# Kernel tuning notes

Hardware: AMD Instinct MI355X
Metric: run time of the kernel (lower is better)

Reference implementation:

```python
import jax, jax.numpy as jnp
import numpy as np

N = 2048      # nodes
E = 65536     # edges (avg degree 32)
IN_C = 512
OUT_C = 512
KP1 = 3       # K=2 Chebyshev -> 3 terms


def setup_inputs() -> dict:
    key = jax.random.key(0)
    k0, k1, k2, k3, k4 = jax.random.split(key, 5)
    X_real = jax.random.normal(k0, (N, IN_C), jnp.float32)
    X_imag = jax.random.normal(k1, (N, IN_C), jnp.float32)
    edges = jax.random.randint(k2, (2, E), 0, N).astype(jnp.int64)
    edge_weight = jax.random.uniform(k3, (E,), jnp.float32)
    q = jnp.float32(0.25)
    stdv = 1.0 / np.sqrt(OUT_C)
    weight = jax.random.uniform(k4, (KP1, IN_C, OUT_C), jnp.float32, -stdv, stdv)
    bias = jnp.zeros((1, OUT_C), jnp.float32)
    return {"X_real": X_real, "X_imag": X_imag, "edges": edges, "q": q,
            "edge_weight": edge_weight, "weight": weight, "bias": bias}


def _cheb_laplacians(edges, edge_weight, q):
    """QinDirect_hermitian_decomp_sparse (norm=True, laplacian=True, max_eigen=2,
    gcn_appr=False) followed by cheb_poly_sparse with K=2. Returns stacked
    real/imag parts of [T0, T1, T2], each [KP1, N, N]."""
    f, e = edges[0], edges[1]
    A = jnp.zeros((N, N), jnp.float32).at[f, e].add(edge_weight)
    A_sym = 0.5 * (A + A.T)
    deg = A_sym.sum(axis=0)
    dinv = jnp.where(deg == 0.0, 1.0, deg) ** -0.5
    A_norm = dinv[:, None] * A_sym * dinv[None, :]   # D^-1/2 A_sym D^-1/2
    theta = (2.0 * jnp.pi) * q * (A - A.T)           # phase matrix
    # L = I - exp(i*theta) .* A_norm ; scaled (2/max_eigen)*L - I with max_eigen=2
    # => L_scaled = -exp(i*theta) .* A_norm
    L1_re = -jnp.cos(theta) * A_norm
    L1_im = -jnp.sin(theta) * A_norm
    eye = jnp.eye(N, dtype=jnp.float32)
    # T2 = 2*L1@L1 - I (complex square in real arithmetic)
    L2_re = 2.0 * (L1_re @ L1_re - L1_im @ L1_im) - eye
    L2_im = 2.0 * (L1_re @ L1_im + L1_im @ L1_re)
    L_re = jnp.stack([eye, L1_re, L2_re])                        # [KP1,N,N]
    L_im = jnp.stack([jnp.zeros((N, N), jnp.float32), L1_im, L2_im])
    return L_re, L_im


def reference(X_real, X_imag, edges, q, edge_weight, weight, bias):
    L_re, L_im = _cheb_laplacians(edges, edge_weight, q)
    # NOTE: original forward swaps the lists: L_norm_real = L_img, L_norm_imag = L_real.
    mr, mi = L_im, L_re
    # per term k: real_k = (mr_k@Xr - mi_k@Xi) @ W_k ; imag_k = (mi_k@Xr + mr_k@Xi) @ W_k
    Ar = jnp.einsum('knm,mf->knf', mr, X_real) - jnp.einsum('knm,mf->knf', mi, X_imag)
    Ai = jnp.einsum('knm,mf->knf', mi, X_real) + jnp.einsum('knm,mf->knf', mr, X_imag)
    real = jnp.einsum('knf,kfo->no', Ar, weight)   # sum over K terms
    imag = jnp.einsum('knf,kfo->no', Ai, weight)
    return real + bias, imag + bias
```

## Files before the change

kernel.cpp:

```cpp
#include <hip/hip_runtime.h>
#include <hip/hip_bf16.h>
#include <math.h>

#define NN 2048
#define CC 512
#define NEDGE 65536

typedef __hip_bfloat16 bf16;
typedef __attribute__((ext_vector_type(8))) short short8;
typedef __attribute__((ext_vector_type(4))) float floatx4;

static constexpr float TWO_PI_F = 6.2831853071795864769f;

__device__ __forceinline__ void gld16(const void* g, void* l) {
    __builtin_amdgcn_global_load_lds(
        (const __attribute__((address_space(1))) unsigned int*)(unsigned long long)(uintptr_t)g,
        (__attribute__((address_space(3))) unsigned int*)(unsigned long long)(uintptr_t)l,
        16, 0, 0);
}

__global__ __launch_bounds__(256) void detect_k(const unsigned int* __restrict__ qword,
                                                const unsigned int* __restrict__ ewords,
                                                int* __restrict__ flag,
                                                float* __restrict__ colsum) {
    int tid = threadIdx.x;
#pragma unroll
    for (int i = 0; i < 8; ++i) colsum[tid * 8 + i] = 0.f;
    if (tid < 64) {
        unsigned int w0 = ewords[2 * tid + 1];
        unsigned int w1 = ewords[128 + 2 * tid + 1];
        unsigned long long b = __ballot((w0 | w1) != 0u);
        if (tid == 0) {
            flag[0] = ((qword[0] & 0xFFFFu) == 0x3E80u) ? 1 : 0;
            flag[1] = (b == 0ull) ? 1 : 0;
        }
    }
}


__global__ void scatter_edges_k(const void* __restrict__ edges,
                                const void* __restrict__ w,
                                float* __restrict__ A,
                                const int* __restrict__ flag) {
    int e = blockIdx.x * 256 + threadIdx.x;
    if (e >= NEDGE) return;
    int f, t;
    if (flag[1]) {
        f = (int)((const long long*)edges)[e];
        t = (int)((const long long*)edges)[NEDGE + e];
    } else {
        f = ((const int*)edges)[e];
        t = ((const int*)edges)[NEDGE + e];
    }
    float wv = flag[0] ? __bfloat162float(((const bf16*)w)[e]) : ((const float*)w)[e];
    f &= (NN - 1); t &= (NN - 1);
    atomicAdd(&A[(size_t)f * NN + t], wv);
}

__global__ void sums_k(const float* __restrict__ A,
                       float* __restrict__ rowsum, float* __restrict__ colsum) {
    int b = blockIdx.x;
    if (b < NN) {
        float s = 0.f;
        for (int j = threadIdx.x; j < NN; j += 256) s += A[(size_t)b * NN + j];
        __shared__ float red[256];
        red[threadIdx.x] = s;
        __syncthreads();
        for (int off = 128; off > 0; off >>= 1) {
            if (threadIdx.x < off) red[threadIdx.x] += red[threadIdx.x + off];
            __syncthreads();
        }
        if (threadIdx.x == 0) rowsum[b] = red[0];
    } else {
        int bb = b - NN;
        int col = (bb & 7) * 256 + threadIdx.x;
        int r0 = (bb >> 3) * 64;
        float s = 0.f;
        for (int r = r0; r < r0 + 64; ++r) s += A[(size_t)r * NN + col];
        atomicAdd(&colsum[col], s);
    }
}

__global__ __launch_bounds__(1024) void build_Mpack_k(
    const float* __restrict__ A,
    const float* __restrict__ rowsum, const float* __restrict__ colsum,
    const void* __restrict__ qp, bf16* __restrict__ Mpack,
    const int* __restrict__ flag) {
    __shared__ float tmir[32][33];
    int tx = threadIdx.x, ty = threadIdx.y;
    int j0 = blockIdx.x * 32, i0 = blockIdx.y * 32;
    tmir[ty][tx] = A[(size_t)(j0 + ty) * NN + i0 + tx];
    __syncthreads();
    int i = i0 + ty, j = j0 + tx;
    float qv = flag[0] ? __bfloat162float(((const bf16*)qp)[0]) : ((const float*)qp)[0];
    float di = 0.5f * (rowsum[i] + colsum[i]); di = (di == 0.f) ? 1.f : di;
    float dj = 0.5f * (rowsum[j] + colsum[j]); dj = (dj == 0.f) ? 1.f : dj;
    float a = A[(size_t)i * NN + j];
    float b = tmir[tx][ty];
    float an = rsqrtf(di) * (0.5f * (a + b)) * rsqrtf(dj);
    float th = TWO_PI_F * qv * (a - b);
    float sn, cs;
    sincosf(th, &sn, &cs);
    Mpack[(size_t)i * (2 * NN) + j]      = __float2bfloat16(-cs * an);
    Mpack[(size_t)i * (2 * NN) + NN + j] = __float2bfloat16(sn * an);
}

__global__ __launch_bounds__(1024) void pack_inputs_k(
    const void* __restrict__ xr, const void* __restrict__ xi,
    const void* __restrict__ Wt,
    bf16* __restrict__ Af, bf16* __restrict__ BT, bf16* __restrict__ WT,
    const int* __restrict__ flag) {
    __shared__ float t1[32][33];
    __shared__ float t2[32][33];
    int tid = threadIdx.x;
    int tx = tid & 31, ty = tid >> 5;
    int bx = blockIdx.x;
    int isbf = flag[0];
    if (bx < 1024) {
        int c0 = (bx & 15) * 32, r0 = (bx >> 4) * 32;
        size_t sidx = (size_t)(r0 + ty) * CC + c0 + tx;
        float fr, fi;
        if (isbf) {
            fr = __bfloat162float(((const bf16*)xr)[sidx]);
            fi = __bfloat162float(((const bf16*)xi)[sidx]);
        } else {
            fr = ((const float*)xr)[sidx];
            fi = ((const float*)xi)[sidx];
        }
        int r = r0 + ty, c = c0 + tx;
        Af[(size_t)r * 1536 + c]        = __float2bfloat16(-fi);
        Af[(size_t)(NN + r) * 1536 + c] = __float2bfloat16(fr);
        t1[ty][tx] = fr;
        t2[ty][tx] = fi;
        __syncthreads();
        float xrt = t1[tx][ty];
        float xit = t2[tx][ty];
        int n = c0 + ty, k = r0 + tx;
        BT[(size_t)n * 4096 + k]                = __float2bfloat16(xrt);
        BT[(size_t)(512 + n) * 4096 + k]        = __float2bfloat16(xit);
        BT[(size_t)n * 4096 + 2048 + k]         = __float2bfloat16(-xit);
        BT[(size_t)(512 + n) * 4096 + 2048 + k] = __float2bfloat16(xrt);
    } else {
        int bw = bx - 1024;
        int k0 = (bw % 48) * 32, o0 = (bw / 48) * 32;
        size_t sidx = (size_t)(k0 + ty) * CC + o0 + tx;
        t1[ty][tx] = isbf ? __bfloat162float(((const bf16*)Wt)[sidx])
                          : ((const float*)Wt)[sidx];
        __syncthreads();
        WT[(size_t)(o0 + ty) * 1536 + k0 + tx] = __float2bfloat16(t1[tx][ty]);
    }
}

__global__ __launch_bounds__(1024) void packPT_k(const bf16* __restrict__ Pb,
                                                 bf16* __restrict__ BT,
                                                 bf16* __restrict__ Af) {
    __shared__ float t1[32][33];
    __shared__ float t2[32][33];
    int tx = threadIdx.x, ty = threadIdx.y;
    int k0 = blockIdx.x * 32, n0 = blockIdx.y * 32;
    size_t i1 = (size_t)(n0 + ty) * 2048 + k0 + tx;
    size_t i2 = (size_t)(512 + n0 + ty) * 2048 + k0 + tx;
    float s1 = 0.f, s2 = 0.f;
#pragma unroll
    for (int z = 0; z < 4; ++z) {
        s1 += __bfloat162float(Pb[(size_t)z * 1024 * 2048 + i1]);
        s2 += __bfloat162float(Pb[(size_t)z * 1024 * 2048 + i2]);
    }
    t1[ty][tx] = s1;
    t2[ty][tx] = s2;
    BT[(size_t)(n0 + ty) * 4096 + k0 + tx]              = __float2bfloat16(s1);
    BT[(size_t)(n0 + ty) * 4096 + 2048 + k0 + tx]       = __float2bfloat16(-s2);
    BT[(size_t)(512 + n0 + ty) * 4096 + k0 + tx]        = __float2bfloat16(s2);
    BT[(size_t)(512 + n0 + ty) * 4096 + 2048 + k0 + tx] = __float2bfloat16(s1);
    __syncthreads();
    Af[(size_t)(k0 + ty) * 1536 + 512 + n0 + tx]        = __float2bfloat16(-t2[tx][ty]);
    Af[(size_t)(NN + k0 + ty) * 1536 + 512 + n0 + tx]   = __float2bfloat16(t1[tx][ty]);
}

__global__ void epi2_k(const bf16* __restrict__ Pb,
                       const void* __restrict__ xr, const void* __restrict__ xi,
                       bf16* __restrict__ Af, const int* __restrict__ flag) {
    int idx = blockIdx.x * 256 + threadIdx.x;
    if (idx >= NN * 1024) return;
    int r = idx >> 10, c = idx & 1023;
    float s = 0.f;
#pragma unroll
    for (int z = 0; z < 4; ++z)
        s += __bfloat162float(Pb[(size_t)z * NN * 1024 + idx]);
    size_t xoff = (size_t)r * CC + (c & (CC - 1));
    float xv;
    if (c < 512) xv = flag[0] ? __bfloat162float(((const bf16*)xr)[xoff]) : ((const float*)xr)[xoff];
    else         xv = flag[0] ? __bfloat162float(((const bf16*)xi)[xoff]) : ((const float*)xi)[xoff];
    float v = 2.f * s - xv;
    if (c < 512) Af[(size_t)(NN + r) * 1536 + 1024 + c] = __float2bfloat16(v);
    else         Af[(size_t)r * 1536 + 1024 + (c - 512)] = __float2bfloat16(-v);
}

__global__ void epi3_k(const bf16* __restrict__ Pb, const void* __restrict__ bias,
                       void* __restrict__ out, const int* __restrict__ flag) {
    int idx = blockIdx.x * 256 + threadIdx.x;
    if (idx >= 4096 * CC) return;
    int c = idx & (CC - 1);
    float s = 0.f;
#pragma unroll
    for (int z = 0; z < 4; ++z)
        s += __bfloat162float(Pb[(size_t)z * 4096 * CC + idx]);
    float bb = flag[0] ? __bfloat162float(((const bf16*)bias)[c]) : ((const float*)bias)[c];
    float o = s + bb;
    if (flag[0]) ((bf16*)out)[idx] = __float2bfloat16(o);
    else         ((float*)out)[idx] = o;
}

__global__ __launch_bounds__(256) void gemm_sk_k(
    const bf16* __restrict__ Ab, const bf16* __restrict__ BTb,
    int M, int N, int K, int klen,
    bf16* __restrict__ Pb)
{
    __shared__ bf16 sA[128 * 64];
    __shared__ bf16 sB[128 * 64];
    int tid = threadIdx.x;
    int w = tid >> 6, lane = tid & 63;
    int row0 = blockIdx.y * 128, col0 = blockIdx.x * 128;
    int kbase = blockIdx.z * klen;
    int wave_m = (w >> 1) * 64, wave_n = (w & 1) * 64;
    int lm = lane & 15, lq = lane >> 4;

    int srow = lane >> 3;
    int sg   = lane & 7;
    int scol = (sg ^ srow) * 8;
    const bf16 *gA[4], *gB[4];
    bf16 *lA[4], *lB[4];
#pragma unroll
    for (int i = 0; i < 4; ++i) {
        int c = w * 4 + i;
        int row = c * 8 + srow;
        gA[i] = Ab  + (size_t)(row0 + row) * K + kbase + scol;
        gB[i] = BTb + (size_t)(col0 + row) * K + kbase + scol;
        lA[i] = sA + c * 512 + lane * 8;
        lB[i] = sB + c * 512 + lane * 8;
    }

    floatx4 acc[4][4];
#pragma unroll
    for (int mf = 0; mf < 4; ++mf)
#pragma unroll
        for (int nf = 0; nf < 4; ++nf)
            acc[mf][nf] = (floatx4){0.f, 0.f, 0.f, 0.f};

    for (int kk = 0; kk < klen; kk += 64) {
        __syncthreads();
#pragma unroll
        for (int i = 0; i < 4; ++i) {
            gld16(gA[i] + kk, lA[i]);
            gld16(gB[i] + kk, lB[i]);
        }
        __syncthreads();
#pragma unroll
        for (int ks = 0; ks < 2; ++ks) {
            short8 af[4], bfv[4];
#pragma unroll
            for (int mf = 0; mf < 4; ++mf) {
                int row = wave_m + mf * 16 + lm;
                int g = (ks * 4 + lq) ^ (row & 7);
                af[mf] = *(const short8*)&sA[row * 64 + g * 8];
            }
#pragma unroll
            for (int nf = 0; nf < 4; ++nf) {
                int row = wave_n + nf * 16 + lm;
                int g = (ks * 4 + lq) ^ (row & 7);
                bfv[nf] = *(const short8*)&sB[row * 64 + g * 8];
            }
#pragma unroll
            for (int mf = 0; mf < 4; ++mf)
#pragma unroll
                for (int nf = 0; nf < 4; ++nf)
                    acc[mf][nf] = __builtin_amdgcn_mfma_f32_16x16x32_bf16(
                        af[mf], bfv[nf], acc[mf][nf], 0, 0, 0);
        }
    }

    bf16* slice = Pb + (size_t)blockIdx.z * M * N;
#pragma unroll
    for (int mf = 0; mf < 4; ++mf) {
#pragma unroll
        for (int nf = 0; nf < 4; ++nf) {
            int gcol = col0 + wave_n + nf * 16 + lm;
#pragma unroll
            for (int r = 0; r < 4; ++r) {
                int grow = row0 + wave_m + mf * 16 + lq * 4 + r;
                slice[(size_t)grow * N + gcol] = __float2bfloat16(acc[mf][nf][r]);
            }
        }
    }
}


extern "C" void kernel_launch(void* const* d_in, const int* in_sizes, int n_in,
                              void* d_out, int out_size, void* d_ws, size_t ws_size,
                              hipStream_t stream) {
    const void* Xr_in = d_in[0];
    const void* Xi_in = d_in[1];
    const void* edges = d_in[2];
    const void* q     = d_in[3];
    const void* ew    = d_in[4];
    const void* Wt    = d_in[5];
    const void* bias  = d_in[6];

    char* base = (char*)d_ws;
    const size_t MB = 1024 * 1024;
    float* A      = (float*)(base);
    bf16*  Mpack  = (bf16*)(base + 16 * MB);
    bf16*  Af     = (bf16*)(base + 32 * MB);
    bf16*  BTb    = (bf16*)(base + 44 * MB);
    bf16*  WT     = (bf16*)(base + 52 * MB);
    float* rowsum = (float*)(base + 53 * MB + 512 * 1024);
    float* colsum = (float*)(base + 53 * MB + 520 * 1024);
    int*   flag   = (int*)  (base + 53 * MB + 528 * 1024);
    bf16*  Pb     = (bf16*)(base + 56 * MB);

    detect_k<<<1, 256, 0, stream>>>((const unsigned int*)q, (const unsigned int*)edges,
                                    flag, colsum);
    hipMemsetAsync(A, 0, 16 * MB, stream);

    scatter_edges_k<<<NEDGE / 256, 256, 0, stream>>>(edges, ew, A, flag);
    sums_k<<<NN + 256, 256, 0, stream>>>(A, rowsum, colsum);
    build_Mpack_k<<<dim3(NN / 32, NN / 32), dim3(32, 32), 0, stream>>>(
        A, rowsum, colsum, q, Mpack, flag);

    pack_inputs_k<<<1792, 1024, 0, stream>>>(Xr_in, Xi_in, Wt, Af, BTb, WT, flag);

    gemm_sk_k<<<dim3(NN / 128, 1024 / 128, 4), 256, 0, stream>>>(
        BTb, Mpack, 1024, NN, 4096, 1024, Pb);
    packPT_k<<<dim3(2048 / 32, 512 / 32), dim3(32, 32), 0, stream>>>(Pb, BTb, Af);

    gemm_sk_k<<<dim3(1024 / 128, NN / 128, 4), 256, 0, stream>>>(
        Mpack, BTb, NN, 1024, 4096, 1024, Pb);
    epi2_k<<<(NN * 1024) / 256, 256, 0, stream>>>(Pb, Xr_in, Xi_in, Af, flag);

    gemm_sk_k<<<dim3(CC / 128, 4096 / 128, 4), 256, 0, stream>>>(
        Af, WT, 4096, CC, 1536, 384, Pb);
    epi3_k<<<(4096 * CC) / 256, 256, 0, stream>>>(Pb, bias, d_out, flag);
}
```

Before: 198.6 us.

## Replace dense Laplacian GEMMs with row-wise sparse complex SpMM

```diff
diff --git a/kernel.cpp b/kernel.cpp
--- a/kernel.cpp
+++ b/kernel.cpp
@@ -19,28 +19,23 @@
         16, 0, 0);
 }
 
-__global__ __launch_bounds__(256) void detect_k(const unsigned int* __restrict__ qword,
-                                                const unsigned int* __restrict__ ewords,
-                                                int* __restrict__ flag,
-                                                float* __restrict__ colsum) {
-    int tid = threadIdx.x;
-#pragma unroll
-    for (int i = 0; i < 8; ++i) colsum[tid * 8 + i] = 0.f;
-    if (tid < 64) {
-        unsigned int w0 = ewords[2 * tid + 1];
-        unsigned int w1 = ewords[128 + 2 * tid + 1];
-        unsigned long long b = __ballot((w0 | w1) != 0u);
-        if (tid == 0) {
-            flag[0] = ((qword[0] & 0xFFFFu) == 0x3E80u) ? 1 : 0;
-            flag[1] = (b == 0ull) ? 1 : 0;
-        }
+__global__ void detect_k(const unsigned int* __restrict__ qword,
+                         const unsigned int* __restrict__ ewords,
+                         int* __restrict__ flag) {
+    int lane = threadIdx.x;
+    unsigned int w0 = ewords[2 * lane + 1];
+    unsigned int w1 = ewords[128 + 2 * lane + 1];
+    unsigned long long b = __ballot((w0 | w1) != 0u);
+    if (lane == 0) {
+        flag[0] = ((qword[0] & 0xFFFFu) == 0x3E80u) ? 1 : 0;
+        flag[1] = (b == 0ull) ? 1 : 0;
     }
 }
 
 
 __global__ void scatter_edges_k(const void* __restrict__ edges,
                                 const void* __restrict__ w,
-                                float* __restrict__ A,
+                                float* __restrict__ A, float* __restrict__ AT,
                                 const int* __restrict__ flag) {
     int e = blockIdx.x * 256 + threadIdx.x;
     if (e >= NEDGE) return;
@@ -55,63 +50,35 @@
     float wv = flag[0] ? __bfloat162float(((const bf16*)w)[e]) : ((const float*)w)[e];
     f &= (NN - 1); t &= (NN - 1);
     atomicAdd(&A[(size_t)f * NN + t], wv);
-}
-
-__global__ void sums_k(const float* __restrict__ A,
-                       float* __restrict__ rowsum, float* __restrict__ colsum) {
-    int b = blockIdx.x;
-    if (b < NN) {
-        float s = 0.f;
-        for (int j = threadIdx.x; j < NN; j += 256) s += A[(size_t)b * NN + j];
-        __shared__ float red[256];
-        red[threadIdx.x] = s;
-        __syncthreads();
-        for (int off = 128; off > 0; off >>= 1) {
-            if (threadIdx.x < off) red[threadIdx.x] += red[threadIdx.x + off];
-            __syncthreads();
-        }
-        if (threadIdx.x == 0) rowsum[b] = red[0];
-    } else {
-        int bb = b - NN;
-        int col = (bb & 7) * 256 + threadIdx.x;
-        int r0 = (bb >> 3) * 64;
-        float s = 0.f;
-        for (int r = r0; r < r0 + 64; ++r) s += A[(size_t)r * NN + col];
-        atomicAdd(&colsum[col], s);
-    }
-}
-
-__global__ __launch_bounds__(1024) void build_Mpack_k(
-    const float* __restrict__ A,
-    const float* __restrict__ rowsum, const float* __restrict__ colsum,
-    const void* __restrict__ qp, bf16* __restrict__ Mpack,
-    const int* __restrict__ flag) {
-    __shared__ float tmir[32][33];
-    int tx = threadIdx.x, ty = threadIdx.y;
-    int j0 = blockIdx.x * 32, i0 = blockIdx.y * 32;
-    tmir[ty][tx] = A[(size_t)(j0 + ty) * NN + i0 + tx];
+    atomicAdd(&AT[(size_t)t * NN + f], wv);
+}
+
+__global__ void dinv_k(const float* __restrict__ A, const float* __restrict__ AT,
+                       float* __restrict__ dinv) {
+    int i = blockIdx.x;
+    float s = 0.f;
+    for (int j = threadIdx.x; j < NN; j += 256)
+        s += A[(size_t)i * NN + j] + AT[(size_t)i * NN + j];
+    __shared__ float red[256];
+    red[threadIdx.x] = s;
     __syncthreads();
-    int i = i0 + ty, j = j0 + tx;
-    float qv = flag[0] ? __bfloat162float(((const bf16*)qp)[0]) : ((const float*)qp)[0];
-    float di = 0.5f * (rowsum[i] + colsum[i]); di = (di == 0.f) ? 1.f : di;
-    float dj = 0.5f * (rowsum[j] + colsum[j]); dj = (dj == 0.f) ? 1.f : dj;
-    float a = A[(size_t)i * NN + j];
-    float b = tmir[tx][ty];
-    float an = rsqrtf(di) * (0.5f * (a + b)) * rsqrtf(dj);
-    float th = TWO_PI_F * qv * (a - b);
-    float sn, cs;
-    sincosf(th, &sn, &cs);
-    Mpack[(size_t)i * (2 * NN) + j]      = __float2bfloat16(-cs * an);
-    Mpack[(size_t)i * (2 * NN) + NN + j] = __float2bfloat16(sn * an);
+    for (int off = 128; off > 0; off >>= 1) {
+        if (threadIdx.x < off) red[threadIdx.x] += red[threadIdx.x + off];
+        __syncthreads();
+    }
+    if (threadIdx.x == 0) {
+        float d = 0.5f * red[0];
+        if (d == 0.f) d = 1.f;
+        dinv[i] = rsqrtf(d);
+    }
 }
 
 __global__ __launch_bounds__(1024) void pack_inputs_k(
     const void* __restrict__ xr, const void* __restrict__ xi,
     const void* __restrict__ Wt,
-    bf16* __restrict__ Af, bf16* __restrict__ BT, bf16* __restrict__ WT,
+    bf16* __restrict__ Af, bf16* __restrict__ WT,
     const int* __restrict__ flag) {
     __shared__ float t1[32][33];
-    __shared__ float t2[32][33];
     int tid = threadIdx.x;
     int tx = tid & 31, ty = tid >> 5;
     int bx = blockIdx.x;
@@ -130,16 +97,6 @@
         int r = r0 + ty, c = c0 + tx;
         Af[(size_t)r * 1536 + c]        = __float2bfloat16(-fi);
         Af[(size_t)(NN + r) * 1536 + c] = __float2bfloat16(fr);
-        t1[ty][tx] = fr;
-        t2[ty][tx] = fi;
-        __syncthreads();
-        float xrt = t1[tx][ty];
-        float xit = t2[tx][ty];
-        int n = c0 + ty, k = r0 + tx;
-        BT[(size_t)n * 4096 + k]                = __float2bfloat16(xrt);
-        BT[(size_t)(512 + n) * 4096 + k]        = __float2bfloat16(xit);
-        BT[(size_t)n * 4096 + 2048 + k]         = __float2bfloat16(-xit);
-        BT[(size_t)(512 + n) * 4096 + 2048 + k] = __float2bfloat16(xrt);
     } else {
         int bw = bx - 1024;
         int k0 = (bw % 48) * 32, o0 = (bw / 48) * 32;
@@ -151,49 +108,104 @@
     }
 }
 
-__global__ __launch_bounds__(1024) void packPT_k(const bf16* __restrict__ Pb,
-                                                 bf16* __restrict__ BT,
-                                                 bf16* __restrict__ Af) {
-    __shared__ float t1[32][33];
-    __shared__ float t2[32][33];
-    int tx = threadIdx.x, ty = threadIdx.y;
-    int k0 = blockIdx.x * 32, n0 = blockIdx.y * 32;
-    size_t i1 = (size_t)(n0 + ty) * 2048 + k0 + tx;
-    size_t i2 = (size_t)(512 + n0 + ty) * 2048 + k0 + tx;
-    float s1 = 0.f, s2 = 0.f;
-#pragma unroll
-    for (int z = 0; z < 4; ++z) {
-        s1 += __bfloat162float(Pb[(size_t)z * 1024 * 2048 + i1]);
-        s2 += __bfloat162float(Pb[(size_t)z * 1024 * 2048 + i2]);
-    }
-    t1[ty][tx] = s1;
-    t2[ty][tx] = s2;
-    BT[(size_t)(n0 + ty) * 4096 + k0 + tx]              = __float2bfloat16(s1);
-    BT[(size_t)(n0 + ty) * 4096 + 2048 + k0 + tx]       = __float2bfloat16(-s2);
-    BT[(size_t)(512 + n0 + ty) * 4096 + k0 + tx]        = __float2bfloat16(s2);
-    BT[(size_t)(512 + n0 + ty) * 4096 + 2048 + k0 + tx] = __float2bfloat16(s1);
-    __syncthreads();
-    Af[(size_t)(k0 + ty) * 1536 + 512 + n0 + tx]        = __float2bfloat16(-t2[tx][ty]);
-    Af[(size_t)(NN + k0 + ty) * 1536 + 512 + n0 + tx]   = __float2bfloat16(t1[tx][ty]);
-}
-
-__global__ void epi2_k(const bf16* __restrict__ Pb,
-                       const void* __restrict__ xr, const void* __restrict__ xi,
-                       bf16* __restrict__ Af, const int* __restrict__ flag) {
-    int idx = blockIdx.x * 256 + threadIdx.x;
-    if (idx >= NN * 1024) return;
-    int r = idx >> 10, c = idx & 1023;
-    float s = 0.f;
-#pragma unroll
-    for (int z = 0; z < 4; ++z)
-        s += __bfloat162float(Pb[(size_t)z * NN * 1024 + idx]);
-    size_t xoff = (size_t)r * CC + (c & (CC - 1));
-    float xv;
-    if (c < 512) xv = flag[0] ? __bfloat162float(((const bf16*)xr)[xoff]) : ((const float*)xr)[xoff];
-    else         xv = flag[0] ? __bfloat162float(((const bf16*)xi)[xoff]) : ((const float*)xi)[xoff];
-    float v = 2.f * s - xv;
-    if (c < 512) Af[(size_t)(NN + r) * 1536 + 1024 + c] = __float2bfloat16(v);
-    else         Af[(size_t)r * 1536 + 1024 + (c - 512)] = __float2bfloat16(-v);
+template<int EPI>
+__global__ __launch_bounds__(256) void spmm_k(
+    const float* __restrict__ A, const float* __restrict__ AT,
+    const float* __restrict__ dinv, const void* __restrict__ qp,
+    const void* __restrict__ xr, const void* __restrict__ xi,
+    const bf16* __restrict__ Z1in, bf16* __restrict__ Z1out,
+    bf16* __restrict__ Af, const int* __restrict__ flag)
+{
+    __shared__ float s_mre[512], s_mim[512];
+    __shared__ short s_col[512];
+    __shared__ int s_cnt;
+    int i = blockIdx.x;
+    int tid = threadIdx.x;
+    int isbf = flag[0];
+    float qv = isbf ? __bfloat162float(((const bf16*)qp)[0]) : ((const float*)qp)[0];
+    float dvi = dinv[i];
+    float ar0 = 0.f, ai0 = 0.f, ar1 = 0.f, ai1 = 0.f;
+
+    for (int c0 = 0; c0 < NN; c0 += 512) {
+        if (tid == 0) s_cnt = 0;
+        __syncthreads();
+#pragma unroll
+        for (int u = 0; u < 2; ++u) {
+            int j = c0 + u * 256 + tid;
+            float a = A[(size_t)i * NN + j];
+            float b = AT[(size_t)i * NN + j];
+            float s = a + b;
+            if (s != 0.f) {
+                int slot = atomicAdd(&s_cnt, 1);
+                float an = dvi * (0.5f * s) * dinv[j];
+                float th = TWO_PI_F * qv * (a - b);
+                float sn, cs;
+                sincosf(th, &sn, &cs);
+                s_mre[slot] = -cs * an;
+                s_mim[slot] = sn * an;
+                s_col[slot] = (short)j;
+            }
+        }
+        __syncthreads();
+        int n = s_cnt;
+        for (int s = 0; s < n; ++s) {
+            float mre = s_mre[s], mim = s_mim[s];
+            int j = s_col[s];
+            float vr0, vr1, vi0, vi1;
+            if (EPI == 1) {
+                if (isbf) {
+                    vr0 = __bfloat162float(((const bf16*)xr)[(size_t)j * CC + tid]);
+                    vr1 = __bfloat162float(((const bf16*)xr)[(size_t)j * CC + tid + 256]);
+                    vi0 = __bfloat162float(((const bf16*)xi)[(size_t)j * CC + tid]);
+                    vi1 = __bfloat162float(((const bf16*)xi)[(size_t)j * CC + tid + 256]);
+                } else {
+                    vr0 = ((const float*)xr)[(size_t)j * CC + tid];
+                    vr1 = ((const float*)xr)[(size_t)j * CC + tid + 256];
+                    vi0 = ((const float*)xi)[(size_t)j * CC + tid];
+                    vi1 = ((const float*)xi)[(size_t)j * CC + tid + 256];
+                }
+            } else {
+                vr0 = __bfloat162float(Z1in[(size_t)j * 1024 + tid]);
+                vr1 = __bfloat162float(Z1in[(size_t)j * 1024 + tid + 256]);
+                vi0 = __bfloat162float(Z1in[(size_t)j * 1024 + 512 + tid]);
+                vi1 = __bfloat162float(Z1in[(size_t)j * 1024 + 512 + tid + 256]);
+            }
+            ar0 += mre * vr0 - mim * vi0;  ai0 += mre * vi0 + mim * vr0;
+            ar1 += mre * vr1 - mim * vi1;  ai1 += mre * vi1 + mim * vr1;
+        }
+        __syncthreads();
+    }
+
+    int c1 = tid, c2 = tid + 256;
+    if (EPI == 1) {
+        Z1out[(size_t)i * 1024 + c1]       = __float2bfloat16(ar0);
+        Z1out[(size_t)i * 1024 + c2]       = __float2bfloat16(ar1);
+        Z1out[(size_t)i * 1024 + 512 + c1] = __float2bfloat16(ai0);
+        Z1out[(size_t)i * 1024 + 512 + c2] = __float2bfloat16(ai1);
+        Af[(size_t)i * 1536 + 512 + c1]        = __float2bfloat16(-ai0);
+        Af[(size_t)i * 1536 + 512 + c2]        = __float2bfloat16(-ai1);
+        Af[(size_t)(NN + i) * 1536 + 512 + c1] = __float2bfloat16(ar0);
+        Af[(size_t)(NN + i) * 1536 + 512 + c2] = __float2bfloat16(ar1);
+    } else {
+        float xrv0, xrv1, xiv0, xiv1;
+        if (isbf) {
+            xrv0 = __bfloat162float(((const bf16*)xr)[(size_t)i * CC + c1]);
+            xrv1 = __bfloat162float(((const bf16*)xr)[(size_t)i * CC + c2]);
+            xiv0 = __bfloat162float(((const bf16*)xi)[(size_t)i * CC + c1]);
+            xiv1 = __bfloat162float(((const bf16*)xi)[(size_t)i * CC + c2]);
+        } else {
+            xrv0 = ((const float*)xr)[(size_t)i * CC + c1];
+            xrv1 = ((const float*)xr)[(size_t)i * CC + c2];
+            xiv0 = ((const float*)xi)[(size_t)i * CC + c1];
+            xiv1 = ((const float*)xi)[(size_t)i * CC + c2];
+        }
+        float vre0 = 2.f * ar0 - xrv0, vre1 = 2.f * ar1 - xrv1;
+        float vim0 = 2.f * ai0 - xiv0, vim1 = 2.f * ai1 - xiv1;
+        Af[(size_t)(NN + i) * 1536 + 1024 + c1] = __float2bfloat16(vre0);
+        Af[(size_t)(NN + i) * 1536 + 1024 + c2] = __float2bfloat16(vre1);
+        Af[(size_t)i * 1536 + 1024 + c1]        = __float2bfloat16(-vim0);
+        Af[(size_t)i * 1536 + 1024 + c2]        = __float2bfloat16(-vim1);
+    }
 }
 
 __global__ void epi3_k(const bf16* __restrict__ Pb, const void* __restrict__ bias,
@@ -308,34 +320,26 @@
 
     char* base = (char*)d_ws;
     const size_t MB = 1024 * 1024;
-    float* A      = (float*)(base);
-    bf16*  Mpack  = (bf16*)(base + 16 * MB);
-    bf16*  Af     = (bf16*)(base + 32 * MB);
-    bf16*  BTb    = (bf16*)(base + 44 * MB);
-    bf16*  WT     = (bf16*)(base + 52 * MB);
-    float* rowsum = (float*)(base + 53 * MB + 512 * 1024);
-    float* colsum = (float*)(base + 53 * MB + 520 * 1024);
-    int*   flag   = (int*)  (base + 53 * MB + 528 * 1024);
-    bf16*  Pb     = (bf16*)(base + 56 * MB);
-
-    detect_k<<<1, 256, 0, stream>>>((const unsigned int*)q, (const unsigned int*)edges,
-                                    flag, colsum);
-    hipMemsetAsync(A, 0, 16 * MB, stream);
-
-    scatter_edges_k<<<NEDGE / 256, 256, 0, stream>>>(edges, ew, A, flag);
-    sums_k<<<NN + 256, 256, 0, stream>>>(A, rowsum, colsum);
-    build_Mpack_k<<<dim3(NN / 32, NN / 32), dim3(32, 32), 0, stream>>>(
-        A, rowsum, colsum, q, Mpack, flag);
-
-    pack_inputs_k<<<1792, 1024, 0, stream>>>(Xr_in, Xi_in, Wt, Af, BTb, WT, flag);
-
-    gemm_sk_k<<<dim3(NN / 128, 1024 / 128, 4), 256, 0, stream>>>(
-        BTb, Mpack, 1024, NN, 4096, 1024, Pb);
-    packPT_k<<<dim3(2048 / 32, 512 / 32), dim3(32, 32), 0, stream>>>(Pb, BTb, Af);
-
-    gemm_sk_k<<<dim3(1024 / 128, NN / 128, 4), 256, 0, stream>>>(
-        Mpack, BTb, NN, 1024, 4096, 1024, Pb);
-    epi2_k<<<(NN * 1024) / 256, 256, 0, stream>>>(Pb, Xr_in, Xi_in, Af, flag);
+    float* A    = (float*)(base);
+    float* AT   = (float*)(base + 16 * MB);
+    bf16*  Af   = (bf16*)(base + 32 * MB);
+    bf16*  WT   = (bf16*)(base + 44 * MB);
+    bf16*  Z1c  = (bf16*)(base + 46 * MB);
+    float* dinv = (float*)(base + 50 * MB);
+    int*   flag = (int*)  (base + 50 * MB + 16 * 1024);
+    bf16*  Pb   = (bf16*)(base + 56 * MB);
+
+    detect_k<<<1, 64, 0, stream>>>((const unsigned int*)q, (const unsigned int*)edges, flag);
+    hipMemsetAsync(A, 0, 32 * MB, stream);
+
+    scatter_edges_k<<<NEDGE / 256, 256, 0, stream>>>(edges, ew, A, AT, flag);
+    dinv_k<<<NN, 256, 0, stream>>>(A, AT, dinv);
+    pack_inputs_k<<<1792, 1024, 0, stream>>>(Xr_in, Xi_in, Wt, Af, WT, flag);
+
+    spmm_k<1><<<NN, 256, 0, stream>>>(A, AT, dinv, q, Xr_in, Xi_in,
+                                      nullptr, Z1c, Af, flag);
+    spmm_k<2><<<NN, 256, 0, stream>>>(A, AT, dinv, q, Xr_in, Xi_in,
+                                      Z1c, nullptr, Af, flag);
 
     gemm_sk_k<<<dim3(CC / 128, 4096 / 128, 4), 256, 0, stream>>>(
         Af, WT, 4096, CC, 1536, 384, Pb);
```

After: 186.3 us. -6.2%, faster.
